# Kernel tuning notes

Measured on AMD Instinct MI355X. Metric: run time of the kernel, lower is better.

## Reference

```python
import jax, jax.numpy as jnp
import numpy as np

N = 50000
E = 800000
IN_DIM = 128
HID = 64
OUT_DIM = 1
NEG_SLOPE = 0.2
EPS = 1e-16


def _glorot(key, shape):
    fan = shape[-1] + (shape[0] if len(shape) > 1 else shape[-1])
    lim = jnp.sqrt(6.0 / fan)
    return jax.random.uniform(key, shape, jnp.float32, -lim, lim)


def setup_inputs() -> dict:
    key = jax.random.key(0)
    ks = jax.random.split(key, 12)
    x = jax.random.normal(ks[0], (N, IN_DIM), jnp.float32)
    edge_index = jax.random.randint(ks[1], (2, E), 0, N, jnp.int64)
    # GATConv layer 1: in=128, out=64, heads=4, concat=True
    W1 = _glorot(ks[2], (4 * HID, IN_DIM))
    att_src1 = _glorot(ks[3], (4, HID))
    att_dst1 = _glorot(ks[4], (4, HID))
    b1 = jnp.zeros((4 * HID,), jnp.float32)
    # GATConv layer 2: in=256, out=64, heads=1, concat=True
    W2 = _glorot(ks[5], (HID, 4 * HID))
    att_src2 = _glorot(ks[6], (1, HID))
    att_dst2 = _glorot(ks[7], (1, HID))
    b2 = jnp.zeros((HID,), jnp.float32)
    # final Linear(hidden, 1)
    fc_w = _glorot(ks[8], (OUT_DIM, HID))
    fc_b = jnp.zeros((OUT_DIM,), jnp.float32)
    return {"x": x, "edge_index": edge_index, "W1": W1, "att_src1": att_src1,
            "att_dst1": att_dst1, "b1": b1, "W2": W2, "att_src2": att_src2,
            "att_dst2": att_dst2, "b2": b2, "fc_w": fc_w, "fc_b": fc_b}


def _gat_layer(x, src, dst, W, att_src, att_dst, bias, heads, out_ch):
    n = x.shape[0]
    xt = (x @ W.T).reshape(n, heads, out_ch)          # [N, H, C]
    a_src = jnp.sum(xt * att_src[None], axis=-1)      # [N, H]
    a_dst = jnp.sum(xt * att_dst[None], axis=-1)      # [N, H]
    e = a_src[src] + a_dst[dst]                       # [E', H]
    e = jnp.where(e > 0, e, NEG_SLOPE * e)            # LeakyReLU(0.2)
    # segment softmax over incoming edges of each dst node
    m = jax.ops.segment_max(e, dst, num_segments=n)
    e = jnp.exp(e - m[dst])
    s = jax.ops.segment_sum(e, dst, num_segments=n)
    alpha = e / (s[dst] + EPS)                        # [E', H]
    msg = xt[src] * alpha[:, :, None]                 # [E', H, C]
    out = jax.ops.segment_sum(msg, dst, num_segments=n)
    return out.reshape(n, heads * out_ch) + bias


def reference(x, edge_index, W1, att_src1, att_dst1, b1,
              W2, att_src2, att_dst2, b2, fc_w, fc_b):
    n = x.shape[0]
    # PyG GATConv default: add self-loops
    loops = jnp.arange(n, dtype=edge_index.dtype)
    src = jnp.concatenate([edge_index[0], loops])
    dst = jnp.concatenate([edge_index[1], loops])
    h = jax.nn.relu(_gat_layer(x, src, dst, W1, att_src1, att_dst1, b1, 4, HID))
    h = jax.nn.relu(_gat_layer(h, src, dst, W2, att_src2, att_dst2, b2, 1, HID))
    logits = h @ fc_w.T + fc_b                        # [N, 1]
    return jax.nn.sigmoid(logits).squeeze()
```

## Files before the change

### kernel.cpp

```cpp
#include <hip/hip_runtime.h>
#include <hip/hip_bf16.h>

#define NN 50000
#define EE 800000
#define ET (NN + EE)
#define SG ((NN + 255) / 256)
#define GB1 ((NN + 63) / 64)

typedef __attribute__((ext_vector_type(8))) short short8;
typedef __attribute__((ext_vector_type(4))) float f32x4;

__device__ __forceinline__ float bf2f(unsigned short u) {
    union { unsigned int i; float f; } v; v.i = ((unsigned int)u) << 16; return v.f;
}
__device__ __forceinline__ unsigned short f2bf(float f) {
    __hip_bfloat16 h = __float2bfloat16(f);
    return *reinterpret_cast<unsigned short*>(&h);
}
__device__ __forceinline__ float lrelu(float e) { return fmaxf(e, 0.2f * e); }


__global__ void k_hist(const int* __restrict__ dst, int* __restrict__ cnt) {
    int i = blockIdx.x * blockDim.x + threadIdx.x;
    if (i < EE) atomicAdd(&cnt[dst[i]], 1);
}

__global__ __launch_bounds__(256) void k_scan1(const int* __restrict__ cnt,
                                               int* __restrict__ tmp, int* __restrict__ bsum) {
    int b = blockIdx.x, t = threadIdx.x, i = b * 256 + t;
    int lane = t & 63, w = t >> 6;
    int v = (i < NN) ? cnt[i] : 0;
    int s = v;
    #pragma unroll
    for (int off = 1; off < 64; off <<= 1) {
        int u = __shfl_up(s, off);
        if (lane >= off) s += u;
    }
    __shared__ int ws[4];
    if (lane == 63) ws[w] = s;
    __syncthreads();
    if (t == 0) {
        int a = 0;
        #pragma unroll
        for (int k = 0; k < 4; k++) { int x = ws[k]; ws[k] = a; a += x; }
        bsum[b] = a;
    }
    __syncthreads();
    s += ws[w];
    if (i < NN) tmp[i] = s;
}

__global__ __launch_bounds__(256) void k_scan2(const int* __restrict__ bsum, int* __restrict__ boff) {
    int t = threadIdx.x, lane = t & 63, w = t >> 6;
    int v = (t < SG) ? bsum[t] : 0;
    int s = v;
    #pragma unroll
    for (int off = 1; off < 64; off <<= 1) {
        int u = __shfl_up(s, off);
        if (lane >= off) s += u;
    }
    __shared__ int ws[4];
    if (lane == 63) ws[w] = s;
    __syncthreads();
    if (t == 0) {
        int a = 0;
        #pragma unroll
        for (int k = 0; k < 4; k++) { int x = ws[k]; ws[k] = a; a += x; }
    }
    __syncthreads();
    s += ws[w];
    if (t < SG) boff[t] = s - v;
}

__global__ void k_scan3_prep(const int* __restrict__ tmp, const int* __restrict__ boff,
                             int* __restrict__ rowptr, int* __restrict__ writeptr,
                             int* __restrict__ csr) {
    int i = blockIdx.x * blockDim.x + threadIdx.x;
    if (i == 0) rowptr[0] = 0;
    if (i < NN) {
        int base = boff[i >> 8];
        int incl = tmp[i] + base + i + 1;
        rowptr[i + 1] = incl;
        int excl = ((i & 255) ? tmp[i - 1] + base : base) + i;
        csr[excl] = i;
        writeptr[i] = excl + 1;
    }
}

template<int K, int N, int NH, bool A_BF16>
__device__ __forceinline__ void gemm_body(
    int bid, const void* __restrict__ Aptr, const float* __restrict__ W,
    const float* __restrict__ atts, const float* __restrict__ attd,
    unsigned short* __restrict__ C, float* __restrict__ as_, float* __restrict__ ad_,
    int M)
{
    constexpr int KU  = K / 8;
    constexpr int KUH = KU / 2;
    constexpr int KC  = K / 32;
    constexpr int NW  = N / 4;
    constexpr int NI  = NW / 16;
    constexpr int ABYTES = 64 * KU * 16;
    constexpr int BBYTES = N * KUH * 16;
    constexpr int SMEM = ABYTES + BBYTES + (NH == 1 ? 2048 : 0);
    __shared__ char smem[SMEM];
    char* Ash = smem;
    char* Bsh = smem + ABYTES;
    unsigned short* Csh = (unsigned short*)smem;
    float* scsh = (float*)(smem + ABYTES + BBYTES);

    int t = threadIdx.x;
    int lane = t & 63, w = t >> 6;
    int colL = lane & 15, quad = lane >> 4;
    int m0 = bid * 64;

    {
        constexpr int CNT = 64 * KU / 256;
        #pragma unroll
        for (int i = 0; i < CNT; i++) {
            int v = t + 256 * i;
            int m = v / KU, u = v % KU;
            int gr = m0 + m; if (gr >= M) gr = M - 1;
            short8 val;
            if (A_BF16) {
                val = *(const short8*)((const unsigned short*)Aptr + (size_t)gr * K + u * 8);
            } else {
                const float* Af = (const float*)Aptr;
                float4 lo = *(const float4*)(Af + (size_t)gr * K + u * 8);
                float4 hi = *(const float4*)(Af + (size_t)gr * K + u * 8 + 4);
                val[0] = (short)f2bf(lo.x); val[1] = (short)f2bf(lo.y);
                val[2] = (short)f2bf(lo.z); val[3] = (short)f2bf(lo.w);
                val[4] = (short)f2bf(hi.x); val[5] = (short)f2bf(hi.y);
                val[6] = (short)f2bf(hi.z); val[7] = (short)f2bf(hi.w);
            }
            *(short8*)(Ash + ((size_t)m * KU + (u ^ (m & 7))) * 16) = val;
        }
    }

    f32x4 acc[4][NI];
    #pragma unroll
    for (int mi = 0; mi < 4; mi++)
        #pragma unroll
        for (int ni = 0; ni < NI; ni++) acc[mi][ni] = (f32x4){0.f, 0.f, 0.f, 0.f};

    #pragma unroll
    for (int kh = 0; kh < 2; kh++) {
        __syncthreads();
        {
            constexpr int CNT = N * KUH / 256;
            #pragma unroll
            for (int i = 0; i < CNT; i++) {
                int v = t + 256 * i;
                int n = v / KUH, uu = v % KUH;
                int u = kh * KUH + uu;
                float4 lo = *(const float4*)(W + (size_t)n * K + u * 8);
                float4 hi = *(const float4*)(W + (size_t)n * K + u * 8 + 4);
                short8 val;
                val[0] = (short)f2bf(lo.x); val[1] = (short)f2bf(lo.y);
                val[2] = (short)f2bf(lo.z); val[3] = (short)f2bf(lo.w);
                val[4] = (short)f2bf(hi.x); val[5] = (short)f2bf(hi.y);
                val[6] = (short)f2bf(hi.z); val[7] = (short)f2bf(hi.w);
                *(short8*)(Bsh + ((size_t)n * KUH + (uu ^ (n & 7))) * 16) = val;
            }
        }
        __syncthreads();
        #pragma unroll
        for (int kcl = 0; kcl < KC / 2; kcl++) {
            int uA = (kh * (KC / 2) + kcl) * 4 + quad;
            int uB = kcl * 4 + quad;
            short8 bf[NI];
            #pragma unroll
            for (int ni = 0; ni < NI; ni++) {
                int n = w * NW + ni * 16 + colL;
                bf[ni] = *(const short8*)(Bsh + ((size_t)n * KUH + (uB ^ (n & 7))) * 16);
            }
            #pragma unroll
            for (int mi = 0; mi < 4; mi++) {
                int m = mi * 16 + colL;
                short8 af = *(const short8*)(Ash + ((size_t)m * KU + (uA ^ (m & 7))) * 16);
                #pragma unroll
                for (int ni = 0; ni < NI; ni++)
                    acc[mi][ni] = __builtin_amdgcn_mfma_f32_16x16x32_bf16(af, bf[ni], acc[mi][ni], 0, 0, 0);
            }
        }
    }
    __syncthreads();

    float asv[NI], adv[NI];
    #pragma unroll
    for (int ni = 0; ni < NI; ni++) {
        int na = (NH == 4) ? (w * 64 + ni * 16 + colL) : (w * 16 + colL);
        asv[ni] = atts[na];
        adv[ni] = attd[na];
    }
    #pragma unroll
    for (int mi = 0; mi < 4; mi++) {
        float ps[4] = {0.f, 0.f, 0.f, 0.f}, pd[4] = {0.f, 0.f, 0.f, 0.f};
        #pragma unroll
        for (int ni = 0; ni < NI; ni++)
            #pragma unroll
            for (int r = 0; r < 4; r++) {
                ps[r] += acc[mi][ni][r] * asv[ni];
                pd[r] += acc[mi][ni][r] * adv[ni];
            }
        #pragma unroll
        for (int off = 1; off < 16; off <<= 1)
            #pragma unroll
            for (int r = 0; r < 4; r++) {
                ps[r] += __shfl_xor(ps[r], off);
                pd[r] += __shfl_xor(pd[r], off);
            }
        if (colL == 0) {
            #pragma unroll
            for (int r = 0; r < 4; r++) {
                int rloc = mi * 16 + quad * 4 + r;
                if (NH == 4) {
                    int row = m0 + rloc;
                    if (row < M) {
                        as_[(size_t)row * 4 + w] = ps[r];
                        ad_[(size_t)row * 4 + w] = pd[r];
                    }
                } else {
                    scsh[(w * 64 + rloc) * 2 + 0] = ps[r];
                    scsh[(w * 64 + rloc) * 2 + 1] = pd[r];
                }
            }
        }
    }

    #pragma unroll
    for (int mi = 0; mi < 4; mi++)
        #pragma unroll
        for (int ni = 0; ni < NI; ni++)
            #pragma unroll
            for (int r = 0; r < 4; r++)
                Csh[(size_t)(mi * 16 + quad * 4 + r) * (N + 8) + w * NW + ni * 16 + colL] =
                    f2bf(acc[mi][ni][r]);
    __syncthreads();

    {
        constexpr int CNT = 64 * (N / 8) / 256;
        #pragma unroll
        for (int i = 0; i < CNT; i++) {
            int v = t + 256 * i;
            int m = v / (N / 8), u = v % (N / 8);
            int row = m0 + m;
            if (row < M)
                *(short8*)(C + (size_t)row * N + u * 8) =
                    *(const short8*)(Csh + (size_t)m * (N + 8) + u * 8);
        }
    }
    if (NH == 1 && t < 64) {
        int row = m0 + t;
        if (row < M) {
            float s = 0.f, d = 0.f;
            #pragma unroll
            for (int ww = 0; ww < 4; ww++) {
                s += scsh[(ww * 64 + t) * 2 + 0];
                d += scsh[(ww * 64 + t) * 2 + 1];
            }
            as_[row] = s;
            ad_[row] = d;
        }
    }
}

template<int K, int N, int NH, bool A_BF16>
__global__ __launch_bounds__(256) void k_gemm_mfma(
    const void* __restrict__ Aptr, const float* __restrict__ W,
    const float* __restrict__ atts, const float* __restrict__ attd,
    unsigned short* __restrict__ C, float* __restrict__ as_, float* __restrict__ ad_,
    int M)
{
    gemm_body<K, N, NH, A_BF16>(blockIdx.x, Aptr, W, atts, attd, C, as_, ad_, M);
}

__global__ __launch_bounds__(256) void k_gemm1_scatter(
    const void* __restrict__ Aptr, const float* __restrict__ W,
    const float* __restrict__ atts, const float* __restrict__ attd,
    unsigned short* __restrict__ C, float* __restrict__ as_, float* __restrict__ ad_,
    int M,
    const int* __restrict__ src, const int* __restrict__ dst,
    int* __restrict__ writeptr, int* __restrict__ csr)
{
    int bid = blockIdx.x;
    int g = bid / 5, r = bid % 5;
    if (r == 0 && g < GB1) {
        gemm_body<128, 256, 4, false>(g, Aptr, W, atts, attd, C, as_, ad_, M);
    } else {
        int ng = (r == 0) ? g : g + 1;
        if (ng > GB1) ng = GB1;
        int sb = bid - ng;
        int i = sb * 256 + threadIdx.x;
        if (i < EE) {
            int pos = atomicAdd(&writeptr[dst[i]], 1);
            csr[pos] = src[i];
        }
    }
}

__global__ __launch_bounds__(256) void k_l1_agg(
    const unsigned short* __restrict__ xt1, const float* __restrict__ as1,
    const float* __restrict__ ad1, const int* __restrict__ rowptr,
    const int* __restrict__ csr, const float* __restrict__ b1,
    unsigned short* __restrict__ h1)
{
    int t = threadIdx.x;
    int lane = t & 63, w = t >> 6;
    int n = blockIdx.x * 4 + w;
    int beg = rowptr[n], deg = rowptr[n + 1] - beg;
    int half = lane >> 5, c = lane & 31, h = c >> 3;
    float adh = ad1[n * 4 + h];
    const char* xb = (const char*)xt1;
    const char* ab = (const char*)as1;
    unsigned co = (unsigned)(c << 4);
    unsigned ho = (unsigned)(h << 2);

    float acc[8] = {0.f, 0.f, 0.f, 0.f, 0.f, 0.f, 0.f, 0.f};
    float esum = 0.f;
    int j = 0;
    for (; j + 8 <= deg; j += 8) {
        int p = beg + j + half * 4;
        int s0 = csr[p], s1 = csr[p + 1], s2 = csr[p + 2], s3 = csr[p + 3];
        float a0 = *(const float*)(ab + ((unsigned)(s0 << 4) + ho));
        float a1 = *(const float*)(ab + ((unsigned)(s1 << 4) + ho));
        float a2 = *(const float*)(ab + ((unsigned)(s2 << 4) + ho));
        float a3 = *(const float*)(ab + ((unsigned)(s3 << 4) + ho));
        short8 r0 = *(const short8*)(xb + ((unsigned)(s0 << 9) + co));
        short8 r1 = *(const short8*)(xb + ((unsigned)(s1 << 9) + co));
        short8 r2 = *(const short8*)(xb + ((unsigned)(s2 << 9) + co));
        short8 r3 = *(const short8*)(xb + ((unsigned)(s3 << 9) + co));
        float e0 = __expf(lrelu(a0 + adh));
        float e1 = __expf(lrelu(a1 + adh));
        float e2 = __expf(lrelu(a2 + adh));
        float e3 = __expf(lrelu(a3 + adh));
        esum += (e0 + e1) + (e2 + e3);
        #pragma unroll
        for (int k = 0; k < 8; k++)
            acc[k] += (bf2f((unsigned short)r0[k]) * e0 + bf2f((unsigned short)r1[k]) * e1)
                    + (bf2f((unsigned short)r2[k]) * e2 + bf2f((unsigned short)r3[k]) * e3);
    }
    if (j + 4 <= deg) {
        int p = beg + j + half * 2;
        int s0 = csr[p], s1 = csr[p + 1];
        float a0 = *(const float*)(ab + ((unsigned)(s0 << 4) + ho));
        float a1 = *(const float*)(ab + ((unsigned)(s1 << 4) + ho));
        short8 r0 = *(const short8*)(xb + ((unsigned)(s0 << 9) + co));
        short8 r1 = *(const short8*)(xb + ((unsigned)(s1 << 9) + co));
        float e0 = __expf(lrelu(a0 + adh));
        float e1 = __expf(lrelu(a1 + adh));
        esum += e0 + e1;
        #pragma unroll
        for (int k = 0; k < 8; k++)
            acc[k] += bf2f((unsigned short)r0[k]) * e0 + bf2f((unsigned short)r1[k]) * e1;
        j += 4;
    }
    for (; j < deg; j += 2) {
        int jj = j + half;
        if (jj < deg) {
            int s = csr[beg + jj];
            float a0 = *(const float*)(ab + ((unsigned)(s << 4) + ho));
            short8 r = *(const short8*)(xb + ((unsigned)(s << 9) + co));
            float e = __expf(lrelu(a0 + adh));
            esum += e;
            #pragma unroll
            for (int k = 0; k < 8; k++) acc[k] += bf2f((unsigned short)r[k]) * e;
        }
    }
    #pragma unroll
    for (int k = 0; k < 8; k++) acc[k] += __shfl_xor(acc[k], 32);
    esum += __shfl_xor(esum, 32);
    if (half == 0) {
        float rs = 1.f / (esum + 1e-16f);
        float4 bl = *(const float4*)(b1 + c * 8);
        float4 bh = *(const float4*)(b1 + c * 8 + 4);
        float bb[8] = {bl.x, bl.y, bl.z, bl.w, bh.x, bh.y, bh.z, bh.w};
        short8 o;
        #pragma unroll
        for (int k = 0; k < 8; k++)
            o[k] = (short)f2bf(fmaxf(acc[k] * rs + bb[k], 0.f));
        *(short8*)(h1 + (size_t)n * 256 + c * 8) = o;
    }
}

__global__ __launch_bounds__(256) void k_l2_agg(
    const unsigned short* __restrict__ xt2, const float* __restrict__ as2,
    const float* __restrict__ ad2, const int* __restrict__ rowptr,
    const int* __restrict__ csr, const float* __restrict__ b2,
    const float* __restrict__ fcw, const float* __restrict__ fcb,
    float* __restrict__ out)
{
    int t = threadIdx.x;
    int lane = t & 63, w = t >> 6;
    int n = blockIdx.x * 4 + w;
    int beg = rowptr[n], deg = rowptr[n + 1] - beg;
    int q = lane >> 4, c = lane & 15;
    float adv = ad2[n];
    const char* xb = (const char*)xt2;
    unsigned co = (unsigned)(c << 3);

    float acc[4] = {0.f, 0.f, 0.f, 0.f};
    float esum = 0.f;
    int j = 0;
    for (; j + 8 <= deg; j += 8) {
        int p = beg + j + q * 2;
        int s0 = csr[p], s1 = csr[p + 1];
        float a0 = as2[s0], a1 = as2[s1];
        uint2 r0 = *(const uint2*)(xb + ((unsigned)(s0 << 7) + co));
        uint2 r1 = *(const uint2*)(xb + ((unsigned)(s1 << 7) + co));
        float e0 = __expf(lrelu(a0 + adv));
        float e1 = __expf(lrelu(a1 + adv));
        esum += e0 + e1;
        acc[0] += bf2f((unsigned short)(r0.x & 0xffff)) * e0 + bf2f((unsigned short)(r1.x & 0xffff)) * e1;
        acc[1] += bf2f((unsigned short)(r0.x >> 16)) * e0 + bf2f((unsigned short)(r1.x >> 16)) * e1;
        acc[2] += bf2f((unsigned short)(r0.y & 0xffff)) * e0 + bf2f((unsigned short)(r1.y & 0xffff)) * e1;
        acc[3] += bf2f((unsigned short)(r0.y >> 16)) * e0 + bf2f((unsigned short)(r1.y >> 16)) * e1;
    }
    for (; j < deg; j += 4) {
        int jj = j + q;
        if (jj < deg) {
            int s = csr[beg + jj];
            float a0 = as2[s];
            uint2 r = *(const uint2*)(xb + ((unsigned)(s << 7) + co));
            float e = __expf(lrelu(a0 + adv));
            esum += e;
            acc[0] += bf2f((unsigned short)(r.x & 0xffff)) * e;
            acc[1] += bf2f((unsigned short)(r.x >> 16)) * e;
            acc[2] += bf2f((unsigned short)(r.y & 0xffff)) * e;
            acc[3] += bf2f((unsigned short)(r.y >> 16)) * e;
        }
    }
    #pragma unroll
    for (int k = 0; k < 4; k++) {
        acc[k] += __shfl_xor(acc[k], 16);
        acc[k] += __shfl_xor(acc[k], 32);
    }
    esum += __shfl_xor(esum, 16);
    esum += __shfl_xor(esum, 32);
    float rs = 1.f / (esum + 1e-16f);
    float4 bv = *(const float4*)(b2 + c * 4);
    float4 fv = *(const float4*)(fcw + c * 4);
    float z = fmaxf(acc[0] * rs + bv.x, 0.f) * fv.x
            + fmaxf(acc[1] * rs + bv.y, 0.f) * fv.y
            + fmaxf(acc[2] * rs + bv.z, 0.f) * fv.z
            + fmaxf(acc[3] * rs + bv.w, 0.f) * fv.w;
    #pragma unroll
    for (int off = 8; off; off >>= 1) z += __shfl_xor(z, off);
    if (lane == 0) out[n] = 1.f / (1.f + __expf(-(z + fcb[0])));
}


extern "C" void kernel_launch(void* const* d_in, const int* in_sizes, int n_in,
                              void* d_out, int out_size, void* d_ws, size_t ws_size,
                              hipStream_t stream) {
    const float* x    = (const float*)d_in[0];
    const int*   ei   = (const int*)d_in[1];
    const float* W1   = (const float*)d_in[2];
    const float* as1w = (const float*)d_in[3];
    const float* ad1w = (const float*)d_in[4];
    const float* b1   = (const float*)d_in[5];
    const float* W2   = (const float*)d_in[6];
    const float* as2w = (const float*)d_in[7];
    const float* ad2w = (const float*)d_in[8];
    const float* b2   = (const float*)d_in[9];
    const float* fcw  = (const float*)d_in[10];
    const float* fcb  = (const float*)d_in[11];
    float* out = (float*)d_out;

    const int* src = ei;
    const int* dst = ei + EE;

    char* base = (char*)d_ws;
    size_t off = 0;
    auto alloc = [&](size_t bytes) -> void* {
        void* p = base + off;
        off = (off + bytes + 255) & ~(size_t)255;
        return p;
    };
    int*   rowptr   = (int*)alloc((NN + 1) * sizeof(int));
    int*   cnt      = (int*)alloc(NN * sizeof(int));
    int*   tmp      = (int*)alloc(NN * sizeof(int));
    int*   bsum     = (int*)alloc(SG * sizeof(int));
    int*   boff     = (int*)alloc(SG * sizeof(int));
    int*   writeptr = (int*)alloc(NN * sizeof(int));
    int*   csr      = (int*)alloc(ET * sizeof(int));
    unsigned short* xt1 = (unsigned short*)alloc((size_t)NN * 256 * sizeof(unsigned short));
    unsigned short* h1  = (unsigned short*)alloc((size_t)NN * 256 * sizeof(unsigned short));
    float* as1      = (float*)alloc(NN * 4 * sizeof(float));
    float* ad1      = (float*)alloc(NN * 4 * sizeof(float));
    float* as2      = (float*)alloc(NN * sizeof(float));
    float* ad2      = (float*)alloc(NN * sizeof(float));
    unsigned short* xt2 = xt1;

    hipMemsetAsync(cnt, 0, NN * sizeof(int), stream);
    k_hist<<<(EE + 255) / 256, 256, 0, stream>>>(dst, cnt);
    k_scan1<<<SG, 256, 0, stream>>>(cnt, tmp, bsum);
    k_scan2<<<1, 256, 0, stream>>>(bsum, boff);
    k_scan3_prep<<<SG, 256, 0, stream>>>(tmp, boff, rowptr, writeptr, csr);

    int fused_blocks = GB1 + (EE + 255) / 256;
    k_gemm1_scatter<<<fused_blocks, 256, 0, stream>>>(
        x, W1, as1w, ad1w, xt1, as1, ad1, NN, src, dst, writeptr, csr);

    k_l1_agg<<<(NN + 3) / 4, 256, 0, stream>>>(xt1, as1, ad1, rowptr, csr, b1, h1);
    k_gemm_mfma<256, 64, 1, true><<<GB1, 256, 0, stream>>>(
        h1, W2, as2w, ad2w, xt2, as2, ad2, NN);
    k_l2_agg<<<(NN + 3) / 4, 256, 0, stream>>>(xt2, as2, ad2, rowptr, csr, b2, fcw, fcb, out);
}
```

Before: 283.1 us.

## Fuse layer-1 aggregation with layer-2 GEMM and software-pipeline gather loops

Layer-1 aggregation now writes each 64-node tile of h1 into shared memory, and the layer-2 MFMA GEMM plus the attention-score reductions run in the same block. This removes the global h1 write and its read-back, along with one launch. Both aggregation loops also prefetch the next batch of neighbor indices and features before computing the current batch. In exchange, the fused kernel launches far fewer blocks (782 instead of 12500), and each wave processes 16 nodes serially, which can reduce latency hiding in the gather-bound aggregation.

```diff
diff --git a/kernel.cpp b/kernel.cpp
--- a/kernel.cpp
+++ b/kernel.cpp
@@ -167,11 +167,11 @@
         for (int kcl = 0; kcl < KC / 2; kcl++) {
             int uA = (kh * (KC / 2) + kcl) * 4 + quad;
             int uB = kcl * 4 + quad;
-            short8 bf[NI];
+            short8 bfr[NI];
             #pragma unroll
             for (int ni = 0; ni < NI; ni++) {
                 int n = w * NW + ni * 16 + colL;
-                bf[ni] = *(const short8*)(Bsh + ((size_t)n * KUH + (uB ^ (n & 7))) * 16);
+                bfr[ni] = *(const short8*)(Bsh + ((size_t)n * KUH + (uB ^ (n & 7))) * 16);
             }
             #pragma unroll
             for (int mi = 0; mi < 4; mi++) {
@@ -179,7 +179,7 @@
                 short8 af = *(const short8*)(Ash + ((size_t)m * KU + (uA ^ (m & 7))) * 16);
                 #pragma unroll
                 for (int ni = 0; ni < NI; ni++)
-                    acc[mi][ni] = __builtin_amdgcn_mfma_f32_16x16x32_bf16(af, bf[ni], acc[mi][ni], 0, 0, 0);
+                    acc[mi][ni] = __builtin_amdgcn_mfma_f32_16x16x32_bf16(af, bfr[ni], acc[mi][ni], 0, 0, 0);
             }
         }
     }
@@ -262,16 +262,6 @@
             ad_[row] = d;
         }
     }
-}
-
-template<int K, int N, int NH, bool A_BF16>
-__global__ __launch_bounds__(256) void k_gemm_mfma(
-    const void* __restrict__ Aptr, const float* __restrict__ W,
-    const float* __restrict__ atts, const float* __restrict__ attd,
-    unsigned short* __restrict__ C, float* __restrict__ as_, float* __restrict__ ad_,
-    int M)
-{
-    gemm_body<K, N, NH, A_BF16>(blockIdx.x, Aptr, W, atts, attd, C, as_, ad_, M);
 }
 
 __global__ __launch_bounds__(256) void k_gemm1_scatter(
@@ -298,87 +288,222 @@
     }
 }
 
-__global__ __launch_bounds__(256) void k_l1_agg(
+__global__ __launch_bounds__(256) void k_l1_gemm2(
     const unsigned short* __restrict__ xt1, const float* __restrict__ as1,
     const float* __restrict__ ad1, const int* __restrict__ rowptr,
     const int* __restrict__ csr, const float* __restrict__ b1,
-    unsigned short* __restrict__ h1)
+    const float* __restrict__ W2, const float* __restrict__ atts2,
+    const float* __restrict__ attd2,
+    unsigned short* __restrict__ xt2, float* __restrict__ as2, float* __restrict__ ad2)
 {
+    __shared__ char smem[64 * 32 * 16 + 2048];
+    char* Ash = smem;
+    float* scsh = (float*)(smem + 64 * 32 * 16);
+    unsigned short* Csh = (unsigned short*)smem;
+
     int t = threadIdx.x;
     int lane = t & 63, w = t >> 6;
-    int n = blockIdx.x * 4 + w;
-    int beg = rowptr[n], deg = rowptr[n + 1] - beg;
     int half = lane >> 5, c = lane & 31, h = c >> 3;
-    float adh = ad1[n * 4 + h];
     const char* xb = (const char*)xt1;
     const char* ab = (const char*)as1;
     unsigned co = (unsigned)(c << 4);
     unsigned ho = (unsigned)(h << 2);
-
-    float acc[8] = {0.f, 0.f, 0.f, 0.f, 0.f, 0.f, 0.f, 0.f};
-    float esum = 0.f;
-    int j = 0;
-    for (; j + 8 <= deg; j += 8) {
-        int p = beg + j + half * 4;
-        int s0 = csr[p], s1 = csr[p + 1], s2 = csr[p + 2], s3 = csr[p + 3];
-        float a0 = *(const float*)(ab + ((unsigned)(s0 << 4) + ho));
-        float a1 = *(const float*)(ab + ((unsigned)(s1 << 4) + ho));
-        float a2 = *(const float*)(ab + ((unsigned)(s2 << 4) + ho));
-        float a3 = *(const float*)(ab + ((unsigned)(s3 << 4) + ho));
-        short8 r0 = *(const short8*)(xb + ((unsigned)(s0 << 9) + co));
-        short8 r1 = *(const short8*)(xb + ((unsigned)(s1 << 9) + co));
-        short8 r2 = *(const short8*)(xb + ((unsigned)(s2 << 9) + co));
-        short8 r3 = *(const short8*)(xb + ((unsigned)(s3 << 9) + co));
-        float e0 = __expf(lrelu(a0 + adh));
-        float e1 = __expf(lrelu(a1 + adh));
-        float e2 = __expf(lrelu(a2 + adh));
-        float e3 = __expf(lrelu(a3 + adh));
-        esum += (e0 + e1) + (e2 + e3);
-        #pragma unroll
-        for (int k = 0; k < 8; k++)
-            acc[k] += (bf2f((unsigned short)r0[k]) * e0 + bf2f((unsigned short)r1[k]) * e1)
-                    + (bf2f((unsigned short)r2[k]) * e2 + bf2f((unsigned short)r3[k]) * e3);
-    }
-    if (j + 4 <= deg) {
-        int p = beg + j + half * 2;
-        int s0 = csr[p], s1 = csr[p + 1];
-        float a0 = *(const float*)(ab + ((unsigned)(s0 << 4) + ho));
-        float a1 = *(const float*)(ab + ((unsigned)(s1 << 4) + ho));
-        short8 r0 = *(const short8*)(xb + ((unsigned)(s0 << 9) + co));
-        short8 r1 = *(const short8*)(xb + ((unsigned)(s1 << 9) + co));
-        float e0 = __expf(lrelu(a0 + adh));
-        float e1 = __expf(lrelu(a1 + adh));
-        esum += e0 + e1;
-        #pragma unroll
-        for (int k = 0; k < 8; k++)
-            acc[k] += bf2f((unsigned short)r0[k]) * e0 + bf2f((unsigned short)r1[k]) * e1;
-        j += 4;
-    }
-    for (; j < deg; j += 2) {
-        int jj = j + half;
-        if (jj < deg) {
-            int s = csr[beg + jj];
-            float a0 = *(const float*)(ab + ((unsigned)(s << 4) + ho));
-            short8 r = *(const short8*)(xb + ((unsigned)(s << 9) + co));
-            float e = __expf(lrelu(a0 + adh));
-            esum += e;
-            #pragma unroll
-            for (int k = 0; k < 8; k++) acc[k] += bf2f((unsigned short)r[k]) * e;
-        }
-    }
-    #pragma unroll
-    for (int k = 0; k < 8; k++) acc[k] += __shfl_xor(acc[k], 32);
-    esum += __shfl_xor(esum, 32);
-    if (half == 0) {
-        float rs = 1.f / (esum + 1e-16f);
-        float4 bl = *(const float4*)(b1 + c * 8);
-        float4 bh = *(const float4*)(b1 + c * 8 + 4);
-        float bb[8] = {bl.x, bl.y, bl.z, bl.w, bh.x, bh.y, bh.z, bh.w};
-        short8 o;
-        #pragma unroll
-        for (int k = 0; k < 8; k++)
-            o[k] = (short)f2bf(fmaxf(acc[k] * rs + bb[k], 0.f));
-        *(short8*)(h1 + (size_t)n * 256 + c * 8) = o;
+    int m0 = blockIdx.x * 64;
+
+    #pragma unroll 1
+    for (int i = 0; i < 16; i++) {
+        int m = w * 16 + i;
+        int n = m0 + m;
+        float acc[8] = {0.f, 0.f, 0.f, 0.f, 0.f, 0.f, 0.f, 0.f};
+        float esum = 0.f;
+        if (n < NN) {
+            int beg = rowptr[n], deg = rowptr[n + 1] - beg;
+            float adh = ad1[(n << 2) + h];
+            int j = 0;
+            if (deg >= 8) {
+                int p = beg + half * 4;
+                int s0 = csr[p], s1 = csr[p + 1], s2 = csr[p + 2], s3 = csr[p + 3];
+                float a0 = *(const float*)(ab + ((unsigned)(s0 << 4) + ho));
+                float a1 = *(const float*)(ab + ((unsigned)(s1 << 4) + ho));
+                float a2 = *(const float*)(ab + ((unsigned)(s2 << 4) + ho));
+                float a3 = *(const float*)(ab + ((unsigned)(s3 << 4) + ho));
+                short8 r0 = *(const short8*)(xb + ((unsigned)(s0 << 9) + co));
+                short8 r1 = *(const short8*)(xb + ((unsigned)(s1 << 9) + co));
+                short8 r2 = *(const short8*)(xb + ((unsigned)(s2 << 9) + co));
+                short8 r3 = *(const short8*)(xb + ((unsigned)(s3 << 9) + co));
+                for (; j + 16 <= deg; j += 8) {
+                    int p2 = beg + j + 8 + half * 4;
+                    int u0 = csr[p2], u1 = csr[p2 + 1], u2 = csr[p2 + 2], u3 = csr[p2 + 3];
+                    float f0 = *(const float*)(ab + ((unsigned)(u0 << 4) + ho));
+                    float f1 = *(const float*)(ab + ((unsigned)(u1 << 4) + ho));
+                    float f2 = *(const float*)(ab + ((unsigned)(u2 << 4) + ho));
+                    float f3 = *(const float*)(ab + ((unsigned)(u3 << 4) + ho));
+                    short8 q0 = *(const short8*)(xb + ((unsigned)(u0 << 9) + co));
+                    short8 q1 = *(const short8*)(xb + ((unsigned)(u1 << 9) + co));
+                    short8 q2 = *(const short8*)(xb + ((unsigned)(u2 << 9) + co));
+                    short8 q3 = *(const short8*)(xb + ((unsigned)(u3 << 9) + co));
+                    float e0 = __expf(lrelu(a0 + adh));
+                    float e1 = __expf(lrelu(a1 + adh));
+                    float e2 = __expf(lrelu(a2 + adh));
+                    float e3 = __expf(lrelu(a3 + adh));
+                    esum += (e0 + e1) + (e2 + e3);
+                    #pragma unroll
+                    for (int k = 0; k < 8; k++)
+                        acc[k] += (bf2f((unsigned short)r0[k]) * e0 + bf2f((unsigned short)r1[k]) * e1)
+                                + (bf2f((unsigned short)r2[k]) * e2 + bf2f((unsigned short)r3[k]) * e3);
+                    a0 = f0; a1 = f1; a2 = f2; a3 = f3;
+                    r0 = q0; r1 = q1; r2 = q2; r3 = q3;
+                }
+                {
+                    float e0 = __expf(lrelu(a0 + adh));
+                    float e1 = __expf(lrelu(a1 + adh));
+                    float e2 = __expf(lrelu(a2 + adh));
+                    float e3 = __expf(lrelu(a3 + adh));
+                    esum += (e0 + e1) + (e2 + e3);
+                    #pragma unroll
+                    for (int k = 0; k < 8; k++)
+                        acc[k] += (bf2f((unsigned short)r0[k]) * e0 + bf2f((unsigned short)r1[k]) * e1)
+                                + (bf2f((unsigned short)r2[k]) * e2 + bf2f((unsigned short)r3[k]) * e3);
+                    j += 8;
+                }
+            }
+            if (j + 4 <= deg) {
+                int p = beg + j + half * 2;
+                int s0 = csr[p], s1 = csr[p + 1];
+                float a0 = *(const float*)(ab + ((unsigned)(s0 << 4) + ho));
+                float a1 = *(const float*)(ab + ((unsigned)(s1 << 4) + ho));
+                short8 r0 = *(const short8*)(xb + ((unsigned)(s0 << 9) + co));
+                short8 r1 = *(const short8*)(xb + ((unsigned)(s1 << 9) + co));
+                float e0 = __expf(lrelu(a0 + adh));
+                float e1 = __expf(lrelu(a1 + adh));
+                esum += e0 + e1;
+                #pragma unroll
+                for (int k = 0; k < 8; k++)
+                    acc[k] += bf2f((unsigned short)r0[k]) * e0 + bf2f((unsigned short)r1[k]) * e1;
+                j += 4;
+            }
+            for (; j < deg; j += 2) {
+                int jj = j + half;
+                if (jj < deg) {
+                    int s = csr[beg + jj];
+                    float a0 = *(const float*)(ab + ((unsigned)(s << 4) + ho));
+                    short8 r = *(const short8*)(xb + ((unsigned)(s << 9) + co));
+                    float e = __expf(lrelu(a0 + adh));
+                    esum += e;
+                    #pragma unroll
+                    for (int k = 0; k < 8; k++) acc[k] += bf2f((unsigned short)r[k]) * e;
+                }
+            }
+        }
+        #pragma unroll
+        for (int k = 0; k < 8; k++) acc[k] += __shfl_xor(acc[k], 32);
+        esum += __shfl_xor(esum, 32);
+        if (half == 0) {
+            short8 o;
+            if (n < NN) {
+                float rs = 1.f / (esum + 1e-16f);
+                float4 bl = *(const float4*)(b1 + c * 8);
+                float4 bh = *(const float4*)(b1 + c * 8 + 4);
+                float bb[8] = {bl.x, bl.y, bl.z, bl.w, bh.x, bh.y, bh.z, bh.w};
+                #pragma unroll
+                for (int k = 0; k < 8; k++)
+                    o[k] = (short)f2bf(fmaxf(acc[k] * rs + bb[k], 0.f));
+            } else {
+                #pragma unroll
+                for (int k = 0; k < 8; k++) o[k] = 0;
+            }
+            *(short8*)(Ash + (((unsigned)(m * 32 + (c ^ (m & 7)))) << 4)) = o;
+        }
+    }
+
+    int colL = lane & 15, quad = lane >> 4;
+    short8 bf[8];
+    {
+        int nrow = w * 16 + colL;
+        const float* wp = W2 + nrow * 256;
+        #pragma unroll
+        for (int kc = 0; kc < 8; kc++) {
+            const float* p = wp + (kc * 4 + quad) * 8;
+            float4 lo = *(const float4*)p;
+            float4 hi = *(const float4*)(p + 4);
+            short8 v;
+            v[0] = (short)f2bf(lo.x); v[1] = (short)f2bf(lo.y);
+            v[2] = (short)f2bf(lo.z); v[3] = (short)f2bf(lo.w);
+            v[4] = (short)f2bf(hi.x); v[5] = (short)f2bf(hi.y);
+            v[6] = (short)f2bf(hi.z); v[7] = (short)f2bf(hi.w);
+            bf[kc] = v;
+        }
+    }
+    __syncthreads();
+
+    f32x4 acc2[4];
+    #pragma unroll
+    for (int mi = 0; mi < 4; mi++) acc2[mi] = (f32x4){0.f, 0.f, 0.f, 0.f};
+    #pragma unroll
+    for (int kc = 0; kc < 8; kc++) {
+        int uA = kc * 4 + quad;
+        #pragma unroll
+        for (int mi = 0; mi < 4; mi++) {
+            int mm = mi * 16 + colL;
+            short8 af = *(const short8*)(Ash + (((unsigned)(mm * 32 + (uA ^ (mm & 7)))) << 4));
+            acc2[mi] = __builtin_amdgcn_mfma_f32_16x16x32_bf16(af, bf[kc], acc2[mi], 0, 0, 0);
+        }
+    }
+
+    {
+        float asv = atts2[w * 16 + colL];
+        float adv = attd2[w * 16 + colL];
+        #pragma unroll
+        for (int mi = 0; mi < 4; mi++) {
+            float ps[4], pd[4];
+            #pragma unroll
+            for (int r = 0; r < 4; r++) { ps[r] = acc2[mi][r] * asv; pd[r] = acc2[mi][r] * adv; }
+            #pragma unroll
+            for (int off = 1; off < 16; off <<= 1)
+                #pragma unroll
+                for (int r = 0; r < 4; r++) {
+                    ps[r] += __shfl_xor(ps[r], off);
+                    pd[r] += __shfl_xor(pd[r], off);
+                }
+            if (colL == 0) {
+                #pragma unroll
+                for (int r = 0; r < 4; r++) {
+                    int rloc = mi * 16 + quad * 4 + r;
+                    scsh[(w * 64 + rloc) * 2 + 0] = ps[r];
+                    scsh[(w * 64 + rloc) * 2 + 1] = pd[r];
+                }
+            }
+        }
+    }
+    __syncthreads();
+
+    #pragma unroll
+    for (int mi = 0; mi < 4; mi++)
+        #pragma unroll
+        for (int r = 0; r < 4; r++)
+            Csh[(size_t)(mi * 16 + quad * 4 + r) * 72 + w * 16 + colL] = f2bf(acc2[mi][r]);
+    if (t < 64) {
+        int row = m0 + t;
+        if (row < NN) {
+            float s = 0.f, d = 0.f;
+            #pragma unroll
+            for (int ww = 0; ww < 4; ww++) {
+                s += scsh[(ww * 64 + t) * 2 + 0];
+                d += scsh[(ww * 64 + t) * 2 + 1];
+            }
+            as2[row] = s;
+            ad2[row] = d;
+        }
+    }
+    __syncthreads();
+    #pragma unroll
+    for (int i2 = 0; i2 < 2; i2++) {
+        int v = t + 256 * i2;
+        int mm = v >> 3, u = v & 7;
+        int row = m0 + mm;
+        if (row < NN)
+            *(short8*)(xt2 + (size_t)row * 64 + u * 8) =
+                *(const short8*)(Csh + (size_t)mm * 72 + u * 8);
     }
 }
 
@@ -401,19 +526,37 @@
     float acc[4] = {0.f, 0.f, 0.f, 0.f};
     float esum = 0.f;
     int j = 0;
-    for (; j + 8 <= deg; j += 8) {
-        int p = beg + j + q * 2;
+    if (deg >= 8) {
+        int p = beg + q * 2;
         int s0 = csr[p], s1 = csr[p + 1];
         float a0 = as2[s0], a1 = as2[s1];
         uint2 r0 = *(const uint2*)(xb + ((unsigned)(s0 << 7) + co));
         uint2 r1 = *(const uint2*)(xb + ((unsigned)(s1 << 7) + co));
-        float e0 = __expf(lrelu(a0 + adv));
-        float e1 = __expf(lrelu(a1 + adv));
-        esum += e0 + e1;
-        acc[0] += bf2f((unsigned short)(r0.x & 0xffff)) * e0 + bf2f((unsigned short)(r1.x & 0xffff)) * e1;
-        acc[1] += bf2f((unsigned short)(r0.x >> 16)) * e0 + bf2f((unsigned short)(r1.x >> 16)) * e1;
-        acc[2] += bf2f((unsigned short)(r0.y & 0xffff)) * e0 + bf2f((unsigned short)(r1.y & 0xffff)) * e1;
-        acc[3] += bf2f((unsigned short)(r0.y >> 16)) * e0 + bf2f((unsigned short)(r1.y >> 16)) * e1;
+        for (; j + 16 <= deg; j += 8) {
+            int p2 = beg + j + 8 + q * 2;
+            int u0 = csr[p2], u1 = csr[p2 + 1];
+            float f0 = as2[u0], f1 = as2[u1];
+            uint2 q0 = *(const uint2*)(xb + ((unsigned)(u0 << 7) + co));
+            uint2 q1 = *(const uint2*)(xb + ((unsigned)(u1 << 7) + co));
+            float e0 = __expf(lrelu(a0 + adv));
+            float e1 = __expf(lrelu(a1 + adv));
+            esum += e0 + e1;
+            acc[0] += bf2f((unsigned short)(r0.x & 0xffff)) * e0 + bf2f((unsigned short)(r1.x & 0xffff)) * e1;
+            acc[1] += bf2f((unsigned short)(r0.x >> 16)) * e0 + bf2f((unsigned short)(r1.x >> 16)) * e1;
+            acc[2] += bf2f((unsigned short)(r0.y & 0xffff)) * e0 + bf2f((unsigned short)(r1.y & 0xffff)) * e1;
+            acc[3] += bf2f((unsigned short)(r0.y >> 16)) * e0 + bf2f((unsigned short)(r1.y >> 16)) * e1;
+            a0 = f0; a1 = f1; r0 = q0; r1 = q1;
+        }
+        {
+            float e0 = __expf(lrelu(a0 + adv));
+            float e1 = __expf(lrelu(a1 + adv));
+            esum += e0 + e1;
+            acc[0] += bf2f((unsigned short)(r0.x & 0xffff)) * e0 + bf2f((unsigned short)(r1.x & 0xffff)) * e1;
+            acc[1] += bf2f((unsigned short)(r0.x >> 16)) * e0 + bf2f((unsigned short)(r1.x >> 16)) * e1;
+            acc[2] += bf2f((unsigned short)(r0.y & 0xffff)) * e0 + bf2f((unsigned short)(r1.y & 0xffff)) * e1;
+            acc[3] += bf2f((unsigned short)(r0.y >> 16)) * e0 + bf2f((unsigned short)(r1.y >> 16)) * e1;
+            j += 8;
+        }
     }
     for (; j < deg; j += 4) {
         int jj = j + q;
@@ -484,12 +627,11 @@
     int*   writeptr = (int*)alloc(NN * sizeof(int));
     int*   csr      = (int*)alloc(ET * sizeof(int));
     unsigned short* xt1 = (unsigned short*)alloc((size_t)NN * 256 * sizeof(unsigned short));
-    unsigned short* h1  = (unsigned short*)alloc((size_t)NN * 256 * sizeof(unsigned short));
+    unsigned short* xt2 = (unsigned short*)alloc((size_t)NN * 64 * sizeof(unsigned short));
     float* as1      = (float*)alloc(NN * 4 * sizeof(float));
     float* ad1      = (float*)alloc(NN * 4 * sizeof(float));
     float* as2      = (float*)alloc(NN * sizeof(float));
     float* ad2      = (float*)alloc(NN * sizeof(float));
-    unsigned short* xt2 = xt1;
 
     hipMemsetAsync(cnt, 0, NN * sizeof(int), stream);
     k_hist<<<(EE + 255) / 256, 256, 0, stream>>>(dst, cnt);
@@ -501,8 +643,8 @@
     k_gemm1_scatter<<<fused_blocks, 256, 0, stream>>>(
         x, W1, as1w, ad1w, xt1, as1, ad1, NN, src, dst, writeptr, csr);
 
-    k_l1_agg<<<(NN + 3) / 4, 256, 0, stream>>>(xt1, as1, ad1, rowptr, csr, b1, h1);
-    k_gemm_mfma<256, 64, 1, true><<<GB1, 256, 0, stream>>>(
-        h1, W2, as2w, ad2w, xt2, as2, ad2, NN);
+    k_l1_gemm2<<<GB1, 256, 0, stream>>>(
+        xt1, as1, ad1, rowptr, csr, b1, W2, as2w, ad2w, xt2, as2, ad2);
+
     k_l2_agg<<<(NN + 3) / 4, 256, 0, stream>>>(xt2, as2, ad2, rowptr, csr, b2, fcw, fcb, out);
 }
```

Result: no change. 281.6 us (-0.5%).
